# Kernel tuning notes

Measured on AMD Instinct MI355X. Metric: run time of the kernel, lower is better.

## Reference

```python
import jax, jax.numpy as jnp
import numpy as np

N_HEAD = 16
HEAD_SIZE = 64  # n_embd // n_head = 1024 // 16


def setup_inputs() -> dict:
    key = jax.random.key(0)
    k1, k2 = jax.random.split(key)
    B, T, C = 2, 2048, 1024
    x = jax.random.normal(k1, (B, T, C), dtype=jnp.float32)
    w_attn = jax.random.normal(k2, (C, 3 * C), dtype=jnp.float32) * (C ** -0.5)
    b_attn = jnp.zeros((3 * C,), dtype=jnp.float32)
    return {"x": x, "w_attn": w_attn, "b_attn": b_attn}


def reference(x, w_attn, b_attn):
    B, T, C = x.shape
    qkv = x @ w_attn + b_attn  # [B, T, 3C]
    q, k, v = jnp.split(qkv, 3, axis=-1)
    # [B, T, H, D] -> [B, H, T, D]
    def heads(t):
        return t.reshape(B, T, N_HEAD, HEAD_SIZE).transpose(0, 2, 1, 3)
    q, k, v = heads(q), heads(k), heads(v)
    scale = HEAD_SIZE ** -0.5
    wei = jnp.einsum('bhqd,bhkd->bhqk', q, k) * scale  # [B, H, T, T]
    causal = jnp.tril(jnp.ones((T, T), dtype=bool))
    wei = jnp.where(causal, wei, -jnp.inf)
    wei = jax.nn.softmax(wei, axis=-1)
    out = jnp.einsum('bhqk,bhkd->bhqd', wei, v)  # [B, H, T, D]
    out = out.transpose(0, 2, 1, 3).reshape(B, T, C)
    return out
```

## Files before the change

### kernel.cpp

```cpp
#include <hip/hip_runtime.h>
#include <hip/hip_bf16.h>

#define BSZ 2
#define SEQ 2048
#define CDIM 1024
#define NHEAD 16
#define HDIM 64
#define M_GEMM (BSZ * SEQ)
#define N_GEMM (3 * CDIM)
#define K_GEMM CDIM
#define QK_PITCH (2 * CDIM)

typedef __attribute__((ext_vector_type(8))) short short8;
typedef __attribute__((ext_vector_type(4))) short short4v;
typedef __attribute__((ext_vector_type(4))) float f32x4;

__device__ __forceinline__ short bf16_rn(float f) {
    unsigned u = __builtin_bit_cast(unsigned, f);
    u += 0x7FFF + ((u >> 16) & 1);
    return (short)(u >> 16);
}

__device__ __forceinline__ void gl2lds16(const short* g, short* l) {
    __builtin_amdgcn_global_load_lds(
        (const __attribute__((address_space(1))) unsigned int*)g,
        (__attribute__((address_space(3))) unsigned int*)l, 16, 0, 0);
}

#define WAITV0() asm volatile("s_waitcnt vmcnt(0)")
#define LGKM0()  asm volatile("s_waitcnt lgkmcnt(0)")
#define SCB()    __builtin_amdgcn_sched_barrier(0)
#define BARRIER() __builtin_amdgcn_s_barrier()

__global__ __launch_bounds__(256) void cvt_fused(const float* __restrict__ X,
                                                 const float* __restrict__ W,
                                                 short* __restrict__ Xb,
                                                 short* __restrict__ WT) {
    const int tid = threadIdx.x;
    if (blockIdx.x < 2048) {
        size_t idx = ((size_t)blockIdx.x * 256 + tid) * 8;
        float4 a = *(const float4*)&X[idx];
        float4 b = *(const float4*)&X[idx + 4];
        short8 o;
        o[0] = bf16_rn(a.x); o[1] = bf16_rn(a.y); o[2] = bf16_rn(a.z); o[3] = bf16_rn(a.w);
        o[4] = bf16_rn(b.x); o[5] = bf16_rn(b.y); o[6] = bf16_rn(b.z); o[7] = bf16_rn(b.w);
        *(short8*)&Xb[idx] = o;
        return;
    }
    __shared__ short T[64][72];
    const int bid = blockIdx.x - 2048;
    const int n0 = (bid % 48) * 64;
    const int k0 = (bid / 48) * 64;
#pragma unroll
    for (int pass = 0; pass < 4; ++pass) {
        int i = pass * 256 + tid;
        int kr = i >> 4;
        int n4 = i & 15;
        float4 v = *(const float4*)&W[(size_t)(k0 + kr) * N_GEMM + n0 + n4 * 4];
        T[n4 * 4 + 0][kr] = bf16_rn(v.x);
        T[n4 * 4 + 1][kr] = bf16_rn(v.y);
        T[n4 * 4 + 2][kr] = bf16_rn(v.z);
        T[n4 * 4 + 3][kr] = bf16_rn(v.w);
    }
    __syncthreads();
#pragma unroll
    for (int pass = 0; pass < 2; ++pass) {
        int o = pass * 256 + tid;
        int nr = o >> 3;
        int c8 = o & 7;
        *(short8*)&WT[(size_t)(n0 + nr) * K_GEMM + k0 + c8 * 8] =
            *(const short8*)&T[nr][c8 * 8];
    }
}

__global__ __launch_bounds__(512, 2) void qkv_gemm_8ph(const short* __restrict__ A,
                                                       const short* __restrict__ Bt,
                                                       const float* __restrict__ bias,
                                                       short* __restrict__ Yqk,
                                                       short* __restrict__ Yv) {
    __shared__ short Asl[32768];
    __shared__ short Bsl[24576];

    const int tid  = threadIdx.x;
    const int w    = tid >> 6;
    const int lane = tid & 63;
    const int l16  = lane & 15;
    const int quad = lane >> 4;
    const int wm   = w >> 2;
    const int wn   = w & 3;
    const int ls   = lane >> 3;
    const int lc   = lane & 7;
    const int fsw  = l16 & 7;

    const int orig = blockIdx.y * 16 + blockIdx.x;
    const int xcd  = orig & 7;
    const int idx  = orig >> 3;
    const int bM   = ((xcd & 1) << 3) + (idx & 7);
    const int bN   = (xcd >> 1) * 4 + (idx >> 3);
    const int m0   = bM << 8;
    const int n0   = bN * 192;

    const short* Ab = A  + (size_t)m0 * K_GEMM;
    const short* Bb = Bt + (size_t)n0 * K_GEMM;

    f32x4 acc[8][3];
#pragma unroll
    for (int i = 0; i < 8; ++i)
#pragma unroll
        for (int j = 0; j < 3; ++j) acc[i][j] = (f32x4){0.f, 0.f, 0.f, 0.f};

    auto stageA = [&](int unit, int tt, int sbuf) {
#pragma unroll
        for (int i = 0; i < 2; ++i) {
            const int u0 = (i * 8 + w) * 8;
            const int tr = (u0 & 63) + ((u0 >> 6) << 7) + unit * 64;
            gl2lds16(Ab + (size_t)(tr + ls) * K_GEMM + tt * 64 + ((lc ^ ls) << 3),
                     &Asl[sbuf * 16384 + tr * 64]);
        }
    };
    auto stageBE = [&](int tt, int sbuf) {
#pragma unroll
        for (int i = 0; i < 2; ++i) {
            const int jb = i * 64 + w * 8;
            const int gr = (jb >> 5) * 48 + (jb & 31);
            gl2lds16(Bb + (size_t)(gr + ls) * K_GEMM + tt * 64 + ((lc ^ ls) << 3),
                     &Bsl[sbuf * 12288 + jb * 64]);
        }
    };
    auto stageBO = [&](int tt, int sbuf) {
        const int t8 = w * 8;
        const int jb = 128 + t8;
        const int gr = (t8 >> 4) * 48 + 32 + (t8 & 15);
        gl2lds16(Bb + (size_t)(gr + ls) * K_GEMM + tt * 64 + ((lc ^ ls) << 3),
                 &Bsl[sbuf * 12288 + jb * 64]);
    };
    auto rdA = [&](int ab, int mi, int ks) -> short8 {
        const int r = wm * 128 + mi * 16 + l16;
        return *(const short8*)&Asl[ab + r * 64 + ((ks * 4 + quad) ^ fsw) * 8];
    };
    auto rdB = [&](int bb, int ni, int ks) -> short8 {
        const int j = (ni < 2) ? (wn * 32 + ni * 16 + l16)
                               : (128 + wn * 16 + l16);
        return *(const short8*)&Bsl[bb + j * 64 + ((ks * 4 + quad) ^ fsw) * 8];
    };

    stageA(0, 0, 0);
    stageBE(0, 0);
    stageA(1, 0, 0);
    stageBO(0, 0);
    WAITV0();
    SCB(); BARRIER(); SCB();

    for (int t = 0; t < 16; ++t) {
        const int buf = t & 1;
        const int sb  = buf ^ 1;
        const int tn  = (t + 1) & 15;
        const int ab  = buf * 16384;
        const int bb  = buf * 12288;

        stageA(0, tn, sb);
        stageBE(tn, sb);
        stageA(1, tn, sb);
        stageBO(tn, sb);

        short8 Af[4][2], Bf[3][2];

#pragma unroll
        for (int mi = 0; mi < 4; ++mi)
#pragma unroll
            for (int ks = 0; ks < 2; ++ks) Af[mi][ks] = rdA(ab, mi, ks);
#pragma unroll
        for (int ni = 0; ni < 3; ++ni)
#pragma unroll
            for (int ks = 0; ks < 2; ++ks) Bf[ni][ks] = rdB(bb, ni, ks);
        LGKM0(); SCB();
        __builtin_amdgcn_s_setprio(1);
#pragma unroll
        for (int mi = 0; mi < 4; ++mi)
#pragma unroll
            for (int ni = 0; ni < 3; ++ni)
#pragma unroll
                for (int ks = 0; ks < 2; ++ks)
                    acc[mi][ni] = __builtin_amdgcn_mfma_f32_16x16x32_bf16(
                        Af[mi][ks], Bf[ni][ks], acc[mi][ni], 0, 0, 0);
        __builtin_amdgcn_s_setprio(0);

#pragma unroll
        for (int mi = 0; mi < 4; ++mi)
#pragma unroll
            for (int ks = 0; ks < 2; ++ks) Af[mi][ks] = rdA(ab, 4 + mi, ks);
        LGKM0(); SCB();
        __builtin_amdgcn_s_setprio(1);
#pragma unroll
        for (int mi = 0; mi < 4; ++mi)
#pragma unroll
            for (int ni = 0; ni < 3; ++ni)
#pragma unroll
                for (int ks = 0; ks < 2; ++ks)
                    acc[4 + mi][ni] = __builtin_amdgcn_mfma_f32_16x16x32_bf16(
                        Af[mi][ks], Bf[ni][ks], acc[4 + mi][ni], 0, 0, 0);
        __builtin_amdgcn_s_setprio(0);

        WAITV0();
        SCB(); BARRIER(); SCB();
    }
    WAITV0();

    const float log2e8 = 0.125f * 1.44269504f;
#pragma unroll
    for (int mi = 0; mi < 8; ++mi) {
#pragma unroll
        for (int ni = 0; ni < 3; ++ni) {
            const int colg = n0 + wn * 48 + ni * 16 + l16;
            const float bb2 = bias[colg];
            if (colg >= 2 * CDIM) {
                const int row0 = m0 + wm * 128 + mi * 16 + quad * 4;
                short4v pk;
#pragma unroll
                for (int r = 0; r < 4; ++r) pk[r] = bf16_rn(acc[mi][ni][r] + bb2);
                *(short4v*)&Yv[(size_t)(colg - 2 * CDIM) * M_GEMM + row0] = pk;
            } else {
                const float qs = (colg < CDIM) ? log2e8 : 1.0f;
#pragma unroll
                for (int r = 0; r < 4; ++r) {
                    const int row = m0 + wm * 128 + mi * 16 + quad * 4 + r;
                    Yqk[(size_t)row * QK_PITCH + colg] =
                        bf16_rn((acc[mi][ni][r] + bb2) * qs);
                }
            }
        }
    }
}

__global__ __launch_bounds__(512) void attn_mfma(const short* __restrict__ qk,
                                                 const short* __restrict__ vT,
                                                 float* __restrict__ out) {
    const int b = blockIdx.z;
    const int h = blockIdx.y;
    const int bx = blockIdx.x;
    const int tid = threadIdx.x;
    const int w = tid >> 6;
    const int ws = w >> 2;
    const int wq = w & 3;
    const int lane = tid & 63;
    const int quad = lane >> 4;
    const int l16 = lane & 15;

    const int qts   = ws ? (31 - bx) : bx;
    const int ktmax = 31 - bx;
    const int q0 = qts * 64;

    __shared__ short Ks[2][64 * 64];
    __shared__ short Vt[2][64 * 64];

    int koff, voff, ldso;
    {
        const int cid = tid;
        const int row = cid >> 3;
        const int hK = (row & 3) | (((row >> 3) & 1) << 2);
        koff = row * QK_PITCH + (((cid & 7) ^ hK)) * 8;
        voff = row * M_GEMM + (((cid & 7) ^ (row & 7))) * 8;
        ldso = (w * 64) * 8;
    }

    const short* qrow = qk + (size_t)(b * SEQ + q0 + wq * 16 + l16) * QK_PITCH + h * HDIM;
    short8 aq[2];
    aq[0] = *(const short8*)(qrow + quad * 8);
    aq[1] = *(const short8*)(qrow + 32 + quad * 8);

    float l_run = 0.f;
    f32x4 o_acc[4];
#pragma unroll
    for (int dt = 0; dt < 4; ++dt) o_acc[dt] = (f32x4){0.f, 0.f, 0.f, 0.f};

    const int qglob = q0 + wq * 16 + l16;
    const short* kb0 = qk + (size_t)(b * SEQ) * QK_PITCH + CDIM + h * HDIM;
    const short* vb0 = vT + (size_t)(h * HDIM) * M_GEMM + b * SEQ;

    const int ksl = l16 & 7;

    const int Fq = ((l16 >> 2) << 3) + (l16 & 3);

    gl2lds16(kb0 + koff, &Ks[0][ldso]);
    gl2lds16(vb0 + voff, &Vt[0][ldso]);
    __syncthreads();

    for (int kt = 0; kt <= ktmax; ++kt) {
        const int cur = kt & 1;

        if (kt < ktmax) {
            const short* kbase = kb0 + (size_t)(kt + 1) * 64 * QK_PITCH;
            const short* vbase = vb0 + (kt + 1) * 64;
            gl2lds16(kbase + koff, &Ks[cur ^ 1][ldso]);
            gl2lds16(vbase + voff, &Vt[cur ^ 1][ldso]);
        }

        if (kt <= qts) {
            const short* KsC = Ks[cur];
            const short* VtC = Vt[cur];

            f32x4 s[4];
#pragma unroll
            for (int nt = 0; nt < 4; ++nt) s[nt] = (f32x4){0.f, 0.f, 0.f, 0.f};
            __builtin_amdgcn_s_setprio(1);
#pragma unroll
            for (int nt = 0; nt < 4; ++nt) {
                const int F  = (nt >> 1) * 32 + (nt & 1) * 4 + Fq;
                const int hF = (F & 3) | (((F >> 3) & 1) << 2);
#pragma unroll
                for (int ks = 0; ks < 2; ++ks) {
                    short8 kf = *(const short8*)&KsC[F * 64 + (((ks * 4 + quad) ^ hF) * 8)];
                    s[nt] = __builtin_amdgcn_mfma_f32_16x16x32_bf16(kf, aq[ks], s[nt], 0, 0, 0);
                }
            }
            __builtin_amdgcn_s_setprio(0);

            short8 pa0, pa1;
            float lsum = 0.f;
            if (kt < qts) {
#pragma unroll
                for (int nt = 0; nt < 4; ++nt)
#pragma unroll
                    for (int r = 0; r < 4; ++r) {
                        float pp = __builtin_amdgcn_exp2f(s[nt][r]);
                        lsum += pp;
                        short pb = bf16_rn(pp);
                        if (nt < 2) pa0[(nt & 1) * 4 + r] = pb;
                        else        pa1[(nt & 1) * 4 + r] = pb;
                    }
            } else {
#pragma unroll
                for (int nt = 0; nt < 4; ++nt)
#pragma unroll
                    for (int r = 0; r < 4; ++r) {
                        int key = kt * 64 + (nt >> 1) * 32 + quad * 8 + (nt & 1) * 4 + r;
                        float pp = __builtin_amdgcn_exp2f(s[nt][r]);
                        pp = (key > qglob) ? 0.f : pp;
                        lsum += pp;
                        short pb = bf16_rn(pp);
                        if (nt < 2) pa0[(nt & 1) * 4 + r] = pb;
                        else        pa1[(nt & 1) * 4 + r] = pb;
                    }
            }
            l_run += lsum;

            __builtin_amdgcn_s_setprio(1);
#pragma unroll
            for (int dt = 0; dt < 4; ++dt)
#pragma unroll
                for (int ks = 0; ks < 2; ++ks) {
                    short8 bv = *(const short8*)&VtC[(dt * 16 + l16) * 64 +
                                                     ((ks * 4 + quad) ^ ksl) * 8];
                    o_acc[dt] = __builtin_amdgcn_mfma_f32_16x16x32_bf16(
                        ks ? pa1 : pa0, bv, o_acc[dt], 0, 0, 0);
                }
            __builtin_amdgcn_s_setprio(0);
        }

        __syncthreads();
    }

    float l = l_run;
    l += __shfl_xor(l, 16);
    l += __shfl_xor(l, 32);
#pragma unroll
    for (int r = 0; r < 4; ++r) {
        float lq = __shfl(l, quad * 4 + r);
        float inv = 1.f / lq;
        int row = q0 + wq * 16 + quad * 4 + r;
        float* optr = out + (size_t)(b * SEQ + row) * CDIM + h * HDIM;
#pragma unroll
        for (int dt = 0; dt < 4; ++dt)
            optr[dt * 16 + l16] = o_acc[dt][r] * inv;
    }
}

extern "C" void kernel_launch(void* const* d_in, const int* in_sizes, int n_in,
                              void* d_out, int out_size, void* d_ws, size_t ws_size,
                              hipStream_t stream) {
    const float* x      = (const float*)d_in[0];
    const float* w_attn = (const float*)d_in[1];
    const float* b_attn = (const float*)d_in[2];
    float* out = (float*)d_out;

    short* qk  = (short*)d_ws;
    short* vT  = (short*)((char*)d_ws + 16777216);
    short* xb  = (short*)((char*)d_ws + 25165824);
    short* wT  = (short*)((char*)d_ws + 33554432);

    cvt_fused<<<2048 + 768, 256, 0, stream>>>(x, w_attn, xb, wT);

    dim3 g1(N_GEMM / 192, M_GEMM / 256);
    qkv_gemm_8ph<<<g1, 512, 0, stream>>>(xb, wT, b_attn, qk, vT);

    dim3 g2(SEQ / 128, NHEAD, BSZ);
    attn_mfma<<<g2, 512, 0, stream>>>(qk, vT, out);
}
```

Measured before the change: 153.9 us.

## Process two query sub-tiles per wave in attention to reuse K/V fragments

The attention kernel drops from 8 to 4 waves per block, and each wave now handles two 16-row query groups (32 rows). K fragments are loaded from LDS once and reused across both groups, and each V fragment feeds two MFMAs, which halves LDS read traffic per FLOP. Each thread now issues two async global-to-LDS copies per tile. Block order along x is reversed for batch 1 to spread causal work across CUs. In exchange, register pressure roughly doubles for accumulators and fragments, and there are fewer waves per block to hide latency.

```diff
diff --git a/kernel.cpp b/kernel.cpp
--- a/kernel.cpp
+++ b/kernel.cpp
@@ -232,57 +232,68 @@
     }
 }
 
-__global__ __launch_bounds__(512) void attn_mfma(const short* __restrict__ qk,
+__global__ __launch_bounds__(256) void attn_mfma(const short* __restrict__ qk,
                                                  const short* __restrict__ vT,
                                                  float* __restrict__ out) {
     const int b = blockIdx.z;
     const int h = blockIdx.y;
     const int bx = blockIdx.x;
+    const int bxe = b ? (15 - bx) : bx;
     const int tid = threadIdx.x;
     const int w = tid >> 6;
-    const int ws = w >> 2;
-    const int wq = w & 3;
+    const int ws = w >> 1;
+    const int wh = w & 1;
     const int lane = tid & 63;
     const int quad = lane >> 4;
     const int l16 = lane & 15;
 
-    const int qts   = ws ? (31 - bx) : bx;
-    const int ktmax = 31 - bx;
+    const int qts   = ws ? (31 - bxe) : bxe;
+    const int ktmax = 31 - bxe;
     const int q0 = qts * 64;
 
     __shared__ short Ks[2][64 * 64];
     __shared__ short Vt[2][64 * 64];
 
-    int koff, voff, ldso;
-    {
-        const int cid = tid;
+    int koff[2], voff[2], ldso[2];
+#pragma unroll
+    for (int p = 0; p < 2; ++p) {
+        const int cid = p * 256 + w * 64 + lane;
         const int row = cid >> 3;
         const int hK = (row & 3) | (((row >> 3) & 1) << 2);
-        koff = row * QK_PITCH + (((cid & 7) ^ hK)) * 8;
-        voff = row * M_GEMM + (((cid & 7) ^ (row & 7))) * 8;
-        ldso = (w * 64) * 8;
-    }
-
-    const short* qrow = qk + (size_t)(b * SEQ + q0 + wq * 16 + l16) * QK_PITCH + h * HDIM;
-    short8 aq[2];
-    aq[0] = *(const short8*)(qrow + quad * 8);
-    aq[1] = *(const short8*)(qrow + 32 + quad * 8);
-
-    float l_run = 0.f;
-    f32x4 o_acc[4];
-#pragma unroll
-    for (int dt = 0; dt < 4; ++dt) o_acc[dt] = (f32x4){0.f, 0.f, 0.f, 0.f};
-
-    const int qglob = q0 + wq * 16 + l16;
+        koff[p] = row * QK_PITCH + (((cid & 7) ^ hK)) * 8;
+        voff[p] = row * M_GEMM + (((cid & 7) ^ (row & 7))) * 8;
+        ldso[p] = (p * 256 + w * 64) * 8;
+    }
+
+    short8 aq[2][2];
+    int qglob[2];
+#pragma unroll
+    for (int g = 0; g < 2; ++g) {
+        const int qrow = q0 + wh * 32 + g * 16 + l16;
+        qglob[g] = qrow;
+        const short* qp = qk + (size_t)(b * SEQ + qrow) * QK_PITCH + h * HDIM;
+        aq[g][0] = *(const short8*)(qp + quad * 8);
+        aq[g][1] = *(const short8*)(qp + 32 + quad * 8);
+    }
+
+    float l_run[2] = {0.f, 0.f};
+    f32x4 o_acc[2][4];
+#pragma unroll
+    for (int g = 0; g < 2; ++g)
+#pragma unroll
+        for (int dt = 0; dt < 4; ++dt) o_acc[g][dt] = (f32x4){0.f, 0.f, 0.f, 0.f};
+
     const short* kb0 = qk + (size_t)(b * SEQ) * QK_PITCH + CDIM + h * HDIM;
     const short* vb0 = vT + (size_t)(h * HDIM) * M_GEMM + b * SEQ;
 
     const int ksl = l16 & 7;
-
     const int Fq = ((l16 >> 2) << 3) + (l16 & 3);
 
-    gl2lds16(kb0 + koff, &Ks[0][ldso]);
-    gl2lds16(vb0 + voff, &Vt[0][ldso]);
+#pragma unroll
+    for (int p = 0; p < 2; ++p) {
+        gl2lds16(kb0 + koff[p], &Ks[0][ldso[p]]);
+        gl2lds16(vb0 + voff[p], &Vt[0][ldso[p]]);
+    }
     __syncthreads();
 
     for (int kt = 0; kt <= ktmax; ++kt) {
@@ -291,58 +302,59 @@
         if (kt < ktmax) {
             const short* kbase = kb0 + (size_t)(kt + 1) * 64 * QK_PITCH;
             const short* vbase = vb0 + (kt + 1) * 64;
-            gl2lds16(kbase + koff, &Ks[cur ^ 1][ldso]);
-            gl2lds16(vbase + voff, &Vt[cur ^ 1][ldso]);
+#pragma unroll
+            for (int p = 0; p < 2; ++p) {
+                gl2lds16(kbase + koff[p], &Ks[cur ^ 1][ldso[p]]);
+                gl2lds16(vbase + voff[p], &Vt[cur ^ 1][ldso[p]]);
+            }
         }
 
         if (kt <= qts) {
             const short* KsC = Ks[cur];
             const short* VtC = Vt[cur];
 
-            f32x4 s[4];
-#pragma unroll
-            for (int nt = 0; nt < 4; ++nt) s[nt] = (f32x4){0.f, 0.f, 0.f, 0.f};
-            __builtin_amdgcn_s_setprio(1);
+            short8 kf[4][2];
 #pragma unroll
             for (int nt = 0; nt < 4; ++nt) {
                 const int F  = (nt >> 1) * 32 + (nt & 1) * 4 + Fq;
                 const int hF = (F & 3) | (((F >> 3) & 1) << 2);
 #pragma unroll
-                for (int ks = 0; ks < 2; ++ks) {
-                    short8 kf = *(const short8*)&KsC[F * 64 + (((ks * 4 + quad) ^ hF) * 8)];
-                    s[nt] = __builtin_amdgcn_mfma_f32_16x16x32_bf16(kf, aq[ks], s[nt], 0, 0, 0);
-                }
+                for (int ks = 0; ks < 2; ++ks)
+                    kf[nt][ks] = *(const short8*)&KsC[F * 64 + (((ks * 4 + quad) ^ hF) * 8)];
             }
-            __builtin_amdgcn_s_setprio(0);
-
-            short8 pa0, pa1;
-            float lsum = 0.f;
-            if (kt < qts) {
+
+            short8 pa[2][2];
+            const bool dg = (kt == qts);
+#pragma unroll
+            for (int g = 0; g < 2; ++g) {
+                f32x4 s[4];
+#pragma unroll
+                for (int nt = 0; nt < 4; ++nt) s[nt] = (f32x4){0.f, 0.f, 0.f, 0.f};
+                __builtin_amdgcn_s_setprio(1);
+#pragma unroll
+                for (int nt = 0; nt < 4; ++nt)
+#pragma unroll
+                    for (int ks = 0; ks < 2; ++ks)
+                        s[nt] = __builtin_amdgcn_mfma_f32_16x16x32_bf16(
+                            kf[nt][ks], aq[g][ks], s[nt], 0, 0, 0);
+                __builtin_amdgcn_s_setprio(0);
+                float lsum = 0.f;
 #pragma unroll
                 for (int nt = 0; nt < 4; ++nt)
 #pragma unroll
                     for (int r = 0; r < 4; ++r) {
                         float pp = __builtin_amdgcn_exp2f(s[nt][r]);
+                        if (dg) {
+                            int key = kt * 64 + (nt >> 1) * 32 + quad * 8 + (nt & 1) * 4 + r;
+                            pp = (key > qglob[g]) ? 0.f : pp;
+                        }
                         lsum += pp;
                         short pb = bf16_rn(pp);
-                        if (nt < 2) pa0[(nt & 1) * 4 + r] = pb;
-                        else        pa1[(nt & 1) * 4 + r] = pb;
+                        if (nt < 2) pa[g][0][(nt & 1) * 4 + r] = pb;
+                        else        pa[g][1][(nt & 1) * 4 + r] = pb;
                     }
-            } else {
-#pragma unroll
-                for (int nt = 0; nt < 4; ++nt)
-#pragma unroll
-                    for (int r = 0; r < 4; ++r) {
-                        int key = kt * 64 + (nt >> 1) * 32 + quad * 8 + (nt & 1) * 4 + r;
-                        float pp = __builtin_amdgcn_exp2f(s[nt][r]);
-                        pp = (key > qglob) ? 0.f : pp;
-                        lsum += pp;
-                        short pb = bf16_rn(pp);
-                        if (nt < 2) pa0[(nt & 1) * 4 + r] = pb;
-                        else        pa1[(nt & 1) * 4 + r] = pb;
-                    }
+                l_run[g] += lsum;
             }
-            l_run += lsum;
 
             __builtin_amdgcn_s_setprio(1);
 #pragma unroll
@@ -351,8 +363,10 @@
                 for (int ks = 0; ks < 2; ++ks) {
                     short8 bv = *(const short8*)&VtC[(dt * 16 + l16) * 64 +
                                                      ((ks * 4 + quad) ^ ksl) * 8];
-                    o_acc[dt] = __builtin_amdgcn_mfma_f32_16x16x32_bf16(
-                        ks ? pa1 : pa0, bv, o_acc[dt], 0, 0, 0);
+#pragma unroll
+                    for (int g = 0; g < 2; ++g)
+                        o_acc[g][dt] = __builtin_amdgcn_mfma_f32_16x16x32_bf16(
+                            pa[g][ks], bv, o_acc[g][dt], 0, 0, 0);
                 }
             __builtin_amdgcn_s_setprio(0);
         }
@@ -360,18 +374,21 @@
         __syncthreads();
     }
 
-    float l = l_run;
-    l += __shfl_xor(l, 16);
-    l += __shfl_xor(l, 32);
-#pragma unroll
-    for (int r = 0; r < 4; ++r) {
-        float lq = __shfl(l, quad * 4 + r);
-        float inv = 1.f / lq;
-        int row = q0 + wq * 16 + quad * 4 + r;
-        float* optr = out + (size_t)(b * SEQ + row) * CDIM + h * HDIM;
-#pragma unroll
-        for (int dt = 0; dt < 4; ++dt)
-            optr[dt * 16 + l16] = o_acc[dt][r] * inv;
+#pragma unroll
+    for (int g = 0; g < 2; ++g) {
+        float l = l_run[g];
+        l += __shfl_xor(l, 16);
+        l += __shfl_xor(l, 32);
+#pragma unroll
+        for (int r = 0; r < 4; ++r) {
+            float lq = __shfl(l, quad * 4 + r);
+            float inv = 1.f / lq;
+            int row = q0 + wh * 32 + g * 16 + quad * 4 + r;
+            float* optr = out + (size_t)(b * SEQ + row) * CDIM + h * HDIM;
+#pragma unroll
+            for (int dt = 0; dt < 4; ++dt)
+                optr[dt * 16 + l16] = o_acc[g][dt][r] * inv;
+        }
     }
 }
 
@@ -394,5 +411,5 @@
     qkv_gemm_8ph<<<g1, 512, 0, stream>>>(xb, wT, b_attn, qk, vT);
 
     dim3 g2(SEQ / 128, NHEAD, BSZ);
-    attn_mfma<<<g2, 512, 0, stream>>>(qk, vT, out);
-}
+    attn_mfma<<<g2, 256, 0, stream>>>(qk, vT, out);
+}
```

Measured after the change: 177.9 us. 15.6% more time.
